# Kernel tuning notes

Hardware: AMD Instinct MI355X
Metric: run time of the kernel (lower is better)

## Reference

```python
import jax, jax.numpy as jnp
import numpy as np

BATCH_SIZE_PER_IM = 512
FG_FRACTION = 0.25
FG_THRESH = 0.5
BG_THRESH_HI = 0.5
BG_THRESH_LO = 0.0
MAX_FG = int(FG_FRACTION * BATCH_SIZE_PER_IM)  # 128


def _rand_boxes(key, shape):
    a = jax.random.uniform(key, shape + (4,), dtype=jnp.float32)
    ymin = jnp.minimum(a[..., 0], a[..., 2])
    ymax = jnp.maximum(a[..., 0], a[..., 2]) + 1e-3
    xmin = jnp.minimum(a[..., 1], a[..., 3])
    xmax = jnp.maximum(a[..., 1], a[..., 3]) + 1e-3
    return jnp.stack([ymin, xmin, ymax, xmax], axis=-1)


def setup_inputs() -> dict:
    key = jax.random.key(0)
    k1, k2, k3, k4 = jax.random.split(key, 4)
    B, N, G = 32, 8192, 128
    boxes = _rand_boxes(k1, (B, N))
    gt_boxes = _rand_boxes(k2, (B, G))
    gt_labels = jax.random.randint(k3, (B, G), 0, 91, dtype=jnp.int32)
    noise = jax.random.uniform(k4, (B, N + G), dtype=jnp.float32)
    return {"boxes": boxes, "gt_boxes": gt_boxes, "gt_labels": gt_labels, "noise": noise}


def _bbox_overlap(boxes, gt_boxes):
    # boxes: [B, M, 4], gt_boxes: [B, G, 4], layout (ymin, xmin, ymax, xmax)
    b_ymin, b_xmin, b_ymax, b_xmax = [boxes[..., i:i + 1] for i in range(4)]  # [B,M,1]
    g_ymin, g_xmin, g_ymax, g_xmax = [gt_boxes[..., i][:, None, :] for i in range(4)]  # [B,1,G]
    i_ymin = jnp.maximum(b_ymin, g_ymin)
    i_xmin = jnp.maximum(b_xmin, g_xmin)
    i_ymax = jnp.minimum(b_ymax, g_ymax)
    i_xmax = jnp.minimum(b_xmax, g_xmax)
    i_area = jnp.maximum(i_ymax - i_ymin, 0.0) * jnp.maximum(i_xmax - i_xmin, 0.0)  # [B,M,G]
    b_area = (b_ymax - b_ymin) * (b_xmax - b_xmin)           # [B,M,1]
    g_area = (g_ymax - g_ymin) * (g_xmax - g_xmin)           # [B,1,G]
    iou = i_area / (b_area + g_area - i_area)
    # padded gt boxes (filled with -1) get IoU = -1
    padding = jnp.logical_and(i_ymin < 0, i_xmin < 0)
    return jnp.where(padding, -1.0, iou)


def reference(boxes, gt_boxes, gt_labels, noise):
    boxes = jax.lax.stop_gradient(boxes)
    all_boxes = jnp.concatenate([boxes, gt_boxes], axis=1)        # [B, M=N+G, 4]
    iou = _bbox_overlap(all_boxes, gt_boxes)                      # [B, M, G]
    max_ov = jnp.max(iou, axis=2)                                 # [B, M]
    p2l = jnp.argmax(iou, axis=2).astype(jnp.int32)               # [B, M]
    box_t = jnp.take_along_axis(gt_boxes, p2l[..., None], axis=1)  # [B, M, 4]
    cls_t = jnp.take_along_axis(gt_labels, p2l, axis=1)           # [B, M]
    pos = max_ov > FG_THRESH
    neg = jnp.logical_and(max_ov >= BG_THRESH_LO, max_ov < BG_THRESH_HI)
    cls_t = jnp.where(neg, 0, cls_t)
    box_t = jnp.where(neg[..., None], 0.0, box_t)
    p2l = jnp.where(neg, 0, p2l)
    # --- balanced fg/bg subsampling (random scores provided in `noise`) ---
    pos_score = jnp.where(pos, noise, -1.0)
    kth = jax.lax.top_k(pos_score, MAX_FG)[0][:, -1:]             # [B,1] threshold
    sel_pos = jnp.logical_and(pos, pos_score >= kth)              # at most MAX_FG fg
    # selected fg get priority band 2+, bg band [0,1), rest -1
    combined = jnp.where(sel_pos, 2.0 + noise, jnp.where(neg, noise, -1.0))
    _, idx = jax.lax.top_k(combined, BATCH_SIZE_PER_IM)           # [B, K]
    rois = jnp.take_along_axis(all_boxes, idx[..., None], axis=1)      # [B, K, 4]
    sample_box_t = jnp.take_along_axis(box_t, idx[..., None], axis=1)  # [B, K, 4]
    sample_cls_t = jnp.take_along_axis(cls_t, idx, axis=1)             # [B, K]
    sample_p2l = jnp.take_along_axis(p2l, idx, axis=1)                 # [B, K]
    return sample_box_t, sample_cls_t, rois, sample_p2l
```

## Files before the change

### kernel.cpp

```cpp
#include <hip/hip_runtime.h>
#include <stdint.h>

#define BATCH 32
#define NBOX 8192
#define NGT 128
#define M (NBOX + NGT)
#define K_OUT 512
#define MAX_FG 128
#define C_CAP 256
#define S_CAP 256
#define U_CAP 1024

#define GSPLIT 2
#define GPER (NGT / GSPLIT)
#define IOU_TPB 256
#define IOU_CB ((M + IOU_TPB - 1) / IOU_TPB)

__device__ __forceinline__ unsigned int bkt1024(float ns) {
    unsigned int u = (unsigned int)(ns * 16777216.0f) >> 14;
    return u > 1023u ? 1023u : u;
}

#define U64KEY(lo, hi) (((unsigned long long)(hi) << 32) | (unsigned long long)(lo))

__global__ __launch_bounds__(256) void iou_kernel(
    const float* __restrict__ boxes,
    const float* __restrict__ gt_boxes,
    unsigned long long* __restrict__ part)
{
    const int s  = blockIdx.x % GSPLIT;
    const int cb = (blockIdx.x / GSPLIT) % IOU_CB;
    const int b  = blockIdx.x / (GSPLIT * IOU_CB);
    const int t  = threadIdx.x;
    const int g0 = s * GPER;

    __shared__ float4 sgt[GPER];
    if (t < GPER)
        sgt[t] = ((const float4*)gt_boxes)[b * NGT + g0 + t];
    __syncthreads();

    const int m = cb * IOU_TPB + t;
    if (m >= M) return;

    float4 bb = (m < NBOX) ? ((const float4*)boxes)[b * NBOX + m]
                           : ((const float4*)gt_boxes)[b * NGT + (m - NBOX)];
    float ba = __fmul_rn(__fsub_rn(bb.z, bb.x), __fsub_rn(bb.w, bb.y));

    float best = -1e30f;
    int bi = 0;
    #pragma unroll 4
    for (int g = 0; g < GPER; ++g) {
        float4 gg = sgt[g];
        float ga = __fmul_rn(__fsub_rn(gg.z, gg.x), __fsub_rn(gg.w, gg.y));
        float iymin = fmaxf(bb.x, gg.x);
        float ixmin = fmaxf(bb.y, gg.y);
        float iymax = fminf(bb.z, gg.z);
        float ixmax = fminf(bb.w, gg.w);
        float ia  = __fmul_rn(fmaxf(__fsub_rn(iymax, iymin), 0.0f),
                              fmaxf(__fsub_rn(ixmax, ixmin), 0.0f));
        float den = __fsub_rn(__fadd_rn(ba, ga), ia);
        float iou = __fdiv_rn(ia, den);
        if (iou > best) { best = iou; bi = g0 + g; }
    }
    part[((size_t)s * BATCH + b) * M + m] =
        U64KEY(127u - (unsigned int)bi, __float_as_uint(best));
}

__device__ __forceinline__ int merged_label(
    const unsigned long long* __restrict__ P0,
    const unsigned long long* __restrict__ P1, int m) {
    unsigned long long ka = P0[m], kb = P1[m];
    unsigned long long kk = ka > kb ? ka : kb;
    return (int)(127u - ((unsigned int)kk & 127u));
}

__global__ __launch_bounds__(1024) void select_kernel(
    const float* __restrict__ boxes,
    const float* __restrict__ gt_boxes,
    const int*   __restrict__ gt_labels,
    const float* __restrict__ noise,
    const unsigned long long* __restrict__ part,
    float* __restrict__ out)
{
    const int b = blockIdx.x;
    const int tid = threadIdx.x;

    __shared__ float sh_ns[M];
    __shared__ unsigned int hist[1024];
    __shared__ unsigned int hist2[1024];
    __shared__ unsigned int bctr[1024];
    __shared__ unsigned short pnmask[M / 8];
    __shared__ float4 sgt[NGT];
    __shared__ int slab[NGT];
    __shared__ float C[C_CAP];
    __shared__ __align__(16) unsigned int   skey[S_CAP + 4];
    __shared__ __align__(16) unsigned short sm[S_CAP + 4];
    __shared__ unsigned int   ukey[U_CAP];
    __shared__ unsigned short um[U_CAP];
    __shared__ unsigned int sh_Bp, sh_needp, sh_cc, sh_n1a, sh_B, sh_kth;

    float* out_bt  = out;
    float* out_cls = out + BATCH * K_OUT * 4;
    float* out_roi = out + BATCH * K_OUT * 5;
    float* out_p2l = out + BATCH * K_OUT * 9;

    const unsigned long long* P0 = part + ((size_t)0 * BATCH + b) * M;
    const unsigned long long* P1 = part + ((size_t)1 * BATCH + b) * M;

    hist[tid] = 0;
    hist2[tid] = 0;
    bctr[tid] = 0;
    if (tid == 0) { sh_cc = 0; sh_n1a = 0; sh_B = 0; sh_kth = 0xBF800000u; }
    if (tid < NGT) {
        sgt[tid]  = ((const float4*)gt_boxes)[b * NGT + tid];
        slab[tid] = gt_labels[b * NGT + tid];
    }
    __syncthreads();

    float f[8];
    unsigned int pb = 0, nb = 0;
    {
        const float4* ns4 = (const float4*)(noise + (size_t)b * M);
        {
            const int c = tid;
            const ulonglong2* a2 = (const ulonglong2*)(P0 + (size_t)c * 8);
            const ulonglong2* b2 = (const ulonglong2*)(P1 + (size_t)c * 8);
            ulonglong2 A0 = a2[0], A1 = a2[1], A2 = a2[2], A3 = a2[3];
            ulonglong2 B0 = b2[0], B1 = b2[1], B2 = b2[2], B3 = b2[3];
            float4 n0 = ns4[2 * c], n1v = ns4[2 * c + 1];
            ((float4*)sh_ns)[2 * c] = n0;
            ((float4*)sh_ns)[2 * c + 1] = n1v;
            f[0] = n0.x; f[1] = n0.y; f[2] = n0.z; f[3] = n0.w;
            f[4] = n1v.x; f[5] = n1v.y; f[6] = n1v.z; f[7] = n1v.w;
            unsigned long long ka[8] = {A0.x, A0.y, A1.x, A1.y,
                                        A2.x, A2.y, A3.x, A3.y};
            unsigned long long kb[8] = {B0.x, B0.y, B1.x, B1.y,
                                        B2.x, B2.y, B3.x, B3.y};
            #pragma unroll
            for (int k = 0; k < 8; ++k) {
                unsigned long long kk = ka[k] > kb[k] ? ka[k] : kb[k];
                unsigned int ub = (unsigned int)(kk >> 32);
                if (ub > 0x3F000000u) {
                    pb |= (1u << k);
                    atomicAdd(&hist2[bkt1024(f[k])], 1u);
                } else if (ub < 0x3F000000u) {
                    nb |= (1u << k);
                    atomicAdd(&hist[bkt1024(f[k])], 1u);
                }
            }
            pnmask[c] = (unsigned short)(pb | (nb << 8));
        }
        if (tid < 16) {
            const int c = 1024 + tid;
            const ulonglong2* a2 = (const ulonglong2*)(P0 + (size_t)c * 8);
            const ulonglong2* b2 = (const ulonglong2*)(P1 + (size_t)c * 8);
            ulonglong2 A0 = a2[0], A1 = a2[1], A2 = a2[2], A3 = a2[3];
            ulonglong2 B0 = b2[0], B1 = b2[1], B2 = b2[2], B3 = b2[3];
            float4 n0 = ns4[2 * c], n1v = ns4[2 * c + 1];
            ((float4*)sh_ns)[2 * c] = n0;
            ((float4*)sh_ns)[2 * c + 1] = n1v;
            float ft[8] = {n0.x, n0.y, n0.z, n0.w, n1v.x, n1v.y, n1v.z, n1v.w};
            unsigned long long ka[8] = {A0.x, A0.y, A1.x, A1.y,
                                        A2.x, A2.y, A3.x, A3.y};
            unsigned long long kb[8] = {B0.x, B0.y, B1.x, B1.y,
                                        B2.x, B2.y, B3.x, B3.y};
            unsigned int pb2 = 0, nb2 = 0;
            #pragma unroll
            for (int k = 0; k < 8; ++k) {
                unsigned long long kk = ka[k] > kb[k] ? ka[k] : kb[k];
                unsigned int ub = (unsigned int)(kk >> 32);
                if (ub > 0x3F000000u) {
                    pb2 |= (1u << k);
                    atomicAdd(&hist2[bkt1024(ft[k])], 1u);
                } else if (ub < 0x3F000000u) {
                    nb2 |= (1u << k);
                    atomicAdd(&hist[bkt1024(ft[k])], 1u);
                }
            }
            pnmask[c] = (unsigned short)(pb2 | (nb2 << 8));
        }
    }
    __syncthreads();

    {
        const int wv = tid >> 6, ln = tid & 63;
        if (wv < 2) {
            unsigned int* H = wv ? hist2 : hist;
            unsigned int s[16];
            #pragma unroll
            for (int k = 0; k < 16; ++k) {
                unsigned int v = H[k * 64 + ln];
                #pragma unroll
                for (int off = 1; off < 64; off <<= 1) {
                    unsigned int o = __shfl_down(v, off, 64);
                    if (ln + off < 64) v += o;
                }
                s[k] = v;
            }
            unsigned int after = 0;
            #pragma unroll
            for (int k = 15; k >= 0; --k) {
                unsigned int tot = __shfl(s[k], 0, 64);
                H[k * 64 + ln] = s[k] + after;
                after += tot;
            }
        }
    }
    __syncthreads();
    const unsigned int nneg = hist[0];
    const unsigned int npos = hist2[0];

    if (npos >= MAX_FG) {
        {
            unsigned int S  = hist2[tid];
            unsigned int Sn = (tid < 1023) ? hist2[tid + 1] : 0;
            if (S >= MAX_FG && Sn < MAX_FG) { sh_Bp = tid; sh_needp = MAX_FG - Sn; }
        }
        __syncthreads();
        const unsigned int Bp = sh_Bp, needp = sh_needp;
        #pragma unroll
        for (int k = 0; k < 8; ++k) {
            if (((pb >> k) & 1u) && bkt1024(f[k]) == Bp) {
                unsigned int slot = atomicAdd(&sh_cc, 1u);
                if (slot < C_CAP) C[slot] = f[k];
            }
        }
        if (tid < 16) {
            unsigned int pb2 = pnmask[1024 + tid] & 0xFFu;
            #pragma unroll
            for (int k = 0; k < 8; ++k) {
                if ((pb2 >> k) & 1u) {
                    float v = sh_ns[(1024 + tid) * 8 + k];
                    if (bkt1024(v) == Bp) {
                        unsigned int slot = atomicAdd(&sh_cc, 1u);
                        if (slot < C_CAP) C[slot] = v;
                    }
                }
            }
        }
        __syncthreads();
        {
            unsigned int cc = min(sh_cc, (unsigned int)C_CAP);
            if (tid < (int)cc) {
                float my = C[tid];
                unsigned int g = 0, e = 0;
                for (unsigned int j = 0; j < cc; ++j) {
                    float v = C[j];
                    g += (v > my) ? 1u : 0u;
                    e += (v == my) ? 1u : 0u;
                }
                if (g < needp && g + e >= needp) sh_kth = __float_as_uint(my);
            }
        }
        __syncthreads();
    }
    const float kthf = __uint_as_float(sh_kth);

    #pragma unroll
    for (int k = 0; k < 8; ++k) {
        if (((pb >> k) & 1u) && f[k] >= kthf) {
            unsigned int slot = atomicAdd(&sh_n1a, 1u);
            if (slot < S_CAP) {
                skey[slot] = __float_as_uint(__fadd_rn(2.0f, f[k]));
                sm[slot]   = (unsigned short)(tid * 8 + k);
            }
        }
    }
    if (tid < 16) {
        unsigned int pb2 = pnmask[1024 + tid] & 0xFFu;
        #pragma unroll
        for (int k = 0; k < 8; ++k) {
            if ((pb2 >> k) & 1u) {
                int m = (1024 + tid) * 8 + k;
                float v = sh_ns[m];
                if (v >= kthf) {
                    unsigned int slot = atomicAdd(&sh_n1a, 1u);
                    if (slot < S_CAP) {
                        skey[slot] = __float_as_uint(__fadd_rn(2.0f, v));
                        sm[slot]   = (unsigned short)m;
                    }
                }
            }
        }
    }
    __syncthreads();
    const unsigned int n1 = min(sh_n1a, (unsigned int)S_CAP);
    const unsigned int k2 = K_OUT - n1;
    const bool enough_neg = (nneg >= k2);

    if (tid < 4) { skey[n1 + tid] = 0u; sm[n1 + tid] = 0xFFFFu; }
    if (enough_neg) {
        unsigned int S  = hist[tid];
        unsigned int Sn = (tid < 1023) ? hist[tid + 1] : 0;
        if (S >= k2 && Sn < k2) sh_B = tid;
    }
    __syncthreads();
    const unsigned int B1 = sh_B;

    if (tid < (int)n1) {
        unsigned int   ki = skey[tid];
        unsigned short mi = sm[tid];
        unsigned int r = 0;
        for (unsigned int j = 0; j < n1; j += 4) {
            uint4   kv = *(const uint4*)&skey[j];
            ushort4 mv = *(const ushort4*)&sm[j];
            r += (kv.x > ki || (kv.x == ki && mv.x < mi)) ? 1u : 0u;
            r += (kv.y > ki || (kv.y == ki && mv.y < mi)) ? 1u : 0u;
            r += (kv.z > ki || (kv.z == ki && mv.z < mi)) ? 1u : 0u;
            r += (kv.w > ki || (kv.w == ki && mv.w < mi)) ? 1u : 0u;
        }
        int mi_ = mi;
        int lbl = merged_label(P0, P1, mi_);
        float4 roi = (mi_ < NBOX) ? ((const float4*)boxes)[b * NBOX + mi_]
                                  : sgt[mi_ - NBOX];
        ((float4*)out_bt)[b * K_OUT + r] = sgt[lbl];
        out_cls[b * K_OUT + r] = (float)slab[lbl];
        ((float4*)out_roi)[b * K_OUT + r] = roi;
        out_p2l[b * K_OUT + r] = (float)lbl;
    }

    #pragma unroll
    for (int k = 0; k < 8; ++k) {
        if ((nb >> k) & 1u) {
            float v = f[k];
            unsigned int be = bkt1024(v);
            if (be >= B1) {
                unsigned int base = (be < 1023) ? hist[be + 1] : 0;
                unsigned int a = base + atomicAdd(&bctr[be], 1u);
                if (a < U_CAP) {
                    ukey[a] = __float_as_uint(v);
                    um[a]   = (unsigned short)(tid * 8 + k);
                }
            }
        }
    }
    if (tid < 16) {
        unsigned int nb2 = (pnmask[1024 + tid] >> 8) & 0xFFu;
        #pragma unroll
        for (int k = 0; k < 8; ++k) {
            if ((nb2 >> k) & 1u) {
                int m = (1024 + tid) * 8 + k;
                float v = sh_ns[m];
                unsigned int be = bkt1024(v);
                if (be >= B1) {
                    unsigned int base = (be < 1023) ? hist[be + 1] : 0;
                    unsigned int a = base + atomicAdd(&bctr[be], 1u);
                    if (a < U_CAP) {
                        ukey[a] = __float_as_uint(v);
                        um[a]   = (unsigned short)m;
                    }
                }
            }
        }
    }
    __syncthreads();

    const unsigned int q = min(hist[B1], (unsigned int)U_CAP);
    for (unsigned int a = tid; a < q; a += 1024) {
        unsigned int   ki = ukey[a];
        unsigned short mi = um[a];
        unsigned int be = bkt1024(__uint_as_float(ki));
        unsigned int base = (be < 1023) ? hist[be + 1] : 0;
        unsigned int end  = min(hist[be], q);
        unsigned int r = base;
        for (unsigned int j = base; j < end; ++j) {
            unsigned int kj = ukey[j];
            if (kj > ki || (kj == ki && um[j] < mi)) ++r;
        }
        if (r < k2) {
            float4 roi = (mi < NBOX) ? ((const float4*)boxes)[b * NBOX + mi]
                                     : sgt[mi - NBOX];
            unsigned int gr = n1 + r;
            ((float4*)out_bt)[b * K_OUT + gr] = make_float4(0.f, 0.f, 0.f, 0.f);
            out_cls[b * K_OUT + gr] = 0.0f;
            ((float4*)out_roi)[b * K_OUT + gr] = roi;
            out_p2l[b * K_OUT + gr] = 0.0f;
        }
    }

    if (!enough_neg) {
        __syncthreads();
        const unsigned int k3 = k2 - nneg;
        for (int m = tid; m < M; m += 1024) {
            if (((pnmask[m >> 3] >> (m & 7)) & 1) && sh_ns[m] < kthf) {
                unsigned int r = 0;
                for (int m2 = 0; m2 < m; ++m2)
                    if (((pnmask[m2 >> 3] >> (m2 & 7)) & 1) && sh_ns[m2] < kthf) ++r;
                if (r < k3) {
                    int lbl = merged_label(P0, P1, m);
                    float4 roi = (m < NBOX) ? ((const float4*)boxes)[b * NBOX + m]
                                            : sgt[m - NBOX];
                    unsigned int gr = n1 + nneg + r;
                    ((float4*)out_bt)[b * K_OUT + gr] = sgt[lbl];
                    out_cls[b * K_OUT + gr] = (float)slab[lbl];
                    ((float4*)out_roi)[b * K_OUT + gr] = roi;
                    out_p2l[b * K_OUT + gr] = (float)lbl;
                }
            }
        }
    }
}

extern "C" void kernel_launch(void* const* d_in, const int* in_sizes, int n_in,
                              void* d_out, int out_size, void* d_ws, size_t ws_size,
                              hipStream_t stream) {
    const float* boxes     = (const float*)d_in[0];
    const float* gt_boxes  = (const float*)d_in[1];
    const int*   gt_labels = (const int*)d_in[2];
    const float* noise     = (const float*)d_in[3];
    unsigned long long* part = (unsigned long long*)d_ws;
    float* out = (float*)d_out;

    iou_kernel<<<BATCH * IOU_CB * GSPLIT, IOU_TPB, 0, stream>>>(boxes, gt_boxes, part);
    select_kernel<<<BATCH, 1024, 0, stream>>>(boxes, gt_boxes, gt_labels, noise,
                                              part, out);
}
```

Before: 108.6 us.

## Move fg/bg classification and histogram building into a wide separate kernel

The per-box merge of the two IoU partial maxima, the fg/bg classification and the noise histograms are moved out of the 32-block select kernel into a new classify kernel spread across the whole GPU. That kernel writes global histograms, with atomics, and per-chunk masks. The iou kernel zeroes the global histograms first. The select kernel then only loads the precomputed histograms and masks, which removes the large shared-memory noise buffer and the serial classification work done by only 32 blocks. In exchange it adds a kernel launch, contended global atomics, and global-memory reads in the rare fallback path.

```diff
diff --git a/kernel.cpp b/kernel.cpp
--- a/kernel.cpp
+++ b/kernel.cpp
@@ -5,6 +5,7 @@
 #define NBOX 8192
 #define NGT 128
 #define M (NBOX + NGT)
+#define NCH (M / 8)
 #define K_OUT 512
 #define MAX_FG 128
 #define C_CAP 256
@@ -16,6 +17,8 @@
 #define IOU_TPB 256
 #define IOU_CB ((M + IOU_TPB - 1) / IOU_TPB)
 
+#define TH_HALF 0x3F000000u
+
 __device__ __forceinline__ unsigned int bkt1024(float ns) {
     unsigned int u = (unsigned int)(ns * 16777216.0f) >> 14;
     return u > 1023u ? 1023u : u;
@@ -26,8 +29,12 @@
 __global__ __launch_bounds__(256) void iou_kernel(
     const float* __restrict__ boxes,
     const float* __restrict__ gt_boxes,
-    unsigned long long* __restrict__ part)
+    unsigned long long* __restrict__ part,
+    unsigned int* __restrict__ hist_g)
 {
+    if (blockIdx.x < 256)
+        hist_g[blockIdx.x * 256 + threadIdx.x] = 0;
+
     const int s  = blockIdx.x % GSPLIT;
     const int cb = (blockIdx.x / GSPLIT) % IOU_CB;
     const int b  = blockIdx.x / (GSPLIT * IOU_CB);
@@ -66,6 +73,55 @@
         U64KEY(127u - (unsigned int)bi, __float_as_uint(best));
 }
 
+__global__ __launch_bounds__(256) void classify_kernel(
+    const unsigned long long* __restrict__ part,
+    const float* __restrict__ noise,
+    unsigned int* __restrict__ hist_g,
+    unsigned short* __restrict__ pn_g)
+{
+    const int c  = blockIdx.x * 256 + threadIdx.x;
+    const int b  = c / NCH;
+    const int cl = c - b * NCH;
+    const int m0 = cl * 8;
+
+    const unsigned long long* P0 = part + ((size_t)0 * BATCH + b) * M + m0;
+    const unsigned long long* P1 = part + ((size_t)1 * BATCH + b) * M + m0;
+    const float4* ns4 = (const float4*)(noise + (size_t)b * M + m0);
+
+    ulonglong2 A0 = ((const ulonglong2*)P0)[0], A1 = ((const ulonglong2*)P0)[1];
+    ulonglong2 A2 = ((const ulonglong2*)P0)[2], A3 = ((const ulonglong2*)P0)[3];
+    ulonglong2 B0 = ((const ulonglong2*)P1)[0], B1 = ((const ulonglong2*)P1)[1];
+    ulonglong2 B2 = ((const ulonglong2*)P1)[2], B3 = ((const ulonglong2*)P1)[3];
+    float4 n0 = ns4[0], n1v = ns4[1];
+
+    unsigned int ha[8] = {
+        (unsigned int)(A0.x >> 32), (unsigned int)(A0.y >> 32),
+        (unsigned int)(A1.x >> 32), (unsigned int)(A1.y >> 32),
+        (unsigned int)(A2.x >> 32), (unsigned int)(A2.y >> 32),
+        (unsigned int)(A3.x >> 32), (unsigned int)(A3.y >> 32)};
+    unsigned int hb[8] = {
+        (unsigned int)(B0.x >> 32), (unsigned int)(B0.y >> 32),
+        (unsigned int)(B1.x >> 32), (unsigned int)(B1.y >> 32),
+        (unsigned int)(B2.x >> 32), (unsigned int)(B2.y >> 32),
+        (unsigned int)(B3.x >> 32), (unsigned int)(B3.y >> 32)};
+    float f[8] = {n0.x, n0.y, n0.z, n0.w, n1v.x, n1v.y, n1v.z, n1v.w};
+
+    unsigned int* hg = hist_g + b * 2048;
+    unsigned int pb = 0, nb = 0;
+    #pragma unroll
+    for (int k = 0; k < 8; ++k) {
+        unsigned int ub = ha[k] > hb[k] ? ha[k] : hb[k];
+        if (ub > TH_HALF) {
+            pb |= (1u << k);
+            atomicAdd(&hg[1024 + bkt1024(f[k])], 1u);
+        } else if (ub < TH_HALF) {
+            nb |= (1u << k);
+            atomicAdd(&hg[bkt1024(f[k])], 1u);
+        }
+    }
+    pn_g[c] = (unsigned short)(pb | (nb << 8));
+}
+
 __device__ __forceinline__ int merged_label(
     const unsigned long long* __restrict__ P0,
     const unsigned long long* __restrict__ P1, int m) {
@@ -80,16 +136,17 @@
     const int*   __restrict__ gt_labels,
     const float* __restrict__ noise,
     const unsigned long long* __restrict__ part,
+    const unsigned int* __restrict__ hist_g,
+    const unsigned short* __restrict__ pn_g,
     float* __restrict__ out)
 {
     const int b = blockIdx.x;
     const int tid = threadIdx.x;
 
-    __shared__ float sh_ns[M];
+    __shared__ float sh_ns_t[128];
     __shared__ unsigned int hist[1024];
     __shared__ unsigned int hist2[1024];
     __shared__ unsigned int bctr[1024];
-    __shared__ unsigned short pnmask[M / 8];
     __shared__ float4 sgt[NGT];
     __shared__ int slab[NGT];
     __shared__ float C[C_CAP];
@@ -106,79 +163,27 @@
 
     const unsigned long long* P0 = part + ((size_t)0 * BATCH + b) * M;
     const unsigned long long* P1 = part + ((size_t)1 * BATCH + b) * M;
-
-    hist[tid] = 0;
-    hist2[tid] = 0;
-    bctr[tid] = 0;
-    if (tid == 0) { sh_cc = 0; sh_n1a = 0; sh_B = 0; sh_kth = 0xBF800000u; }
-    if (tid < NGT) {
-        sgt[tid]  = ((const float4*)gt_boxes)[b * NGT + tid];
-        slab[tid] = gt_labels[b * NGT + tid];
-    }
-    __syncthreads();
+    const unsigned short* pn = pn_g + (size_t)b * NCH;
 
     float f[8];
-    unsigned int pb = 0, nb = 0;
+    unsigned int pb, nb;
     {
         const float4* ns4 = (const float4*)(noise + (size_t)b * M);
-        {
-            const int c = tid;
-            const ulonglong2* a2 = (const ulonglong2*)(P0 + (size_t)c * 8);
-            const ulonglong2* b2 = (const ulonglong2*)(P1 + (size_t)c * 8);
-            ulonglong2 A0 = a2[0], A1 = a2[1], A2 = a2[2], A3 = a2[3];
-            ulonglong2 B0 = b2[0], B1 = b2[1], B2 = b2[2], B3 = b2[3];
-            float4 n0 = ns4[2 * c], n1v = ns4[2 * c + 1];
-            ((float4*)sh_ns)[2 * c] = n0;
-            ((float4*)sh_ns)[2 * c + 1] = n1v;
-            f[0] = n0.x; f[1] = n0.y; f[2] = n0.z; f[3] = n0.w;
-            f[4] = n1v.x; f[5] = n1v.y; f[6] = n1v.z; f[7] = n1v.w;
-            unsigned long long ka[8] = {A0.x, A0.y, A1.x, A1.y,
-                                        A2.x, A2.y, A3.x, A3.y};
-            unsigned long long kb[8] = {B0.x, B0.y, B1.x, B1.y,
-                                        B2.x, B2.y, B3.x, B3.y};
-            #pragma unroll
-            for (int k = 0; k < 8; ++k) {
-                unsigned long long kk = ka[k] > kb[k] ? ka[k] : kb[k];
-                unsigned int ub = (unsigned int)(kk >> 32);
-                if (ub > 0x3F000000u) {
-                    pb |= (1u << k);
-                    atomicAdd(&hist2[bkt1024(f[k])], 1u);
-                } else if (ub < 0x3F000000u) {
-                    nb |= (1u << k);
-                    atomicAdd(&hist[bkt1024(f[k])], 1u);
-                }
-            }
-            pnmask[c] = (unsigned short)(pb | (nb << 8));
-        }
-        if (tid < 16) {
-            const int c = 1024 + tid;
-            const ulonglong2* a2 = (const ulonglong2*)(P0 + (size_t)c * 8);
-            const ulonglong2* b2 = (const ulonglong2*)(P1 + (size_t)c * 8);
-            ulonglong2 A0 = a2[0], A1 = a2[1], A2 = a2[2], A3 = a2[3];
-            ulonglong2 B0 = b2[0], B1 = b2[1], B2 = b2[2], B3 = b2[3];
-            float4 n0 = ns4[2 * c], n1v = ns4[2 * c + 1];
-            ((float4*)sh_ns)[2 * c] = n0;
-            ((float4*)sh_ns)[2 * c + 1] = n1v;
-            float ft[8] = {n0.x, n0.y, n0.z, n0.w, n1v.x, n1v.y, n1v.z, n1v.w};
-            unsigned long long ka[8] = {A0.x, A0.y, A1.x, A1.y,
-                                        A2.x, A2.y, A3.x, A3.y};
-            unsigned long long kb[8] = {B0.x, B0.y, B1.x, B1.y,
-                                        B2.x, B2.y, B3.x, B3.y};
-            unsigned int pb2 = 0, nb2 = 0;
-            #pragma unroll
-            for (int k = 0; k < 8; ++k) {
-                unsigned long long kk = ka[k] > kb[k] ? ka[k] : kb[k];
-                unsigned int ub = (unsigned int)(kk >> 32);
-                if (ub > 0x3F000000u) {
-                    pb2 |= (1u << k);
-                    atomicAdd(&hist2[bkt1024(ft[k])], 1u);
-                } else if (ub < 0x3F000000u) {
-                    nb2 |= (1u << k);
-                    atomicAdd(&hist[bkt1024(ft[k])], 1u);
-                }
-            }
-            pnmask[c] = (unsigned short)(pb2 | (nb2 << 8));
-        }
+        float4 n0 = ns4[2 * tid], n1v = ns4[2 * tid + 1];
+        f[0] = n0.x; f[1] = n0.y; f[2] = n0.z; f[3] = n0.w;
+        f[4] = n1v.x; f[5] = n1v.y; f[6] = n1v.z; f[7] = n1v.w;
+        unsigned int pnv = pn[tid];
+        pb = pnv & 0xFFu;
+        nb = (pnv >> 8) & 0xFFu;
+        hist[tid]  = hist_g[b * 2048 + tid];
+        hist2[tid] = hist_g[b * 2048 + 1024 + tid];
+        bctr[tid] = 0;
+        if (tid < 128) sh_ns_t[tid] = noise[(size_t)b * M + NBOX + tid];
+        if (tid < NGT) {
+            sgt[tid]  = ((const float4*)gt_boxes)[b * NGT + tid];
+            slab[tid] = gt_labels[b * NGT + tid];
+        }
+        if (tid == 0) { sh_cc = 0; sh_n1a = 0; sh_B = 0; sh_kth = 0xBF800000u; }
     }
     __syncthreads();
 
@@ -226,11 +231,11 @@
             }
         }
         if (tid < 16) {
-            unsigned int pb2 = pnmask[1024 + tid] & 0xFFu;
+            unsigned int pb2 = pn[1024 + tid] & 0xFFu;
             #pragma unroll
             for (int k = 0; k < 8; ++k) {
                 if ((pb2 >> k) & 1u) {
-                    float v = sh_ns[(1024 + tid) * 8 + k];
+                    float v = sh_ns_t[tid * 8 + k];
                     if (bkt1024(v) == Bp) {
                         unsigned int slot = atomicAdd(&sh_cc, 1u);
                         if (slot < C_CAP) C[slot] = v;
@@ -267,17 +272,16 @@
         }
     }
     if (tid < 16) {
-        unsigned int pb2 = pnmask[1024 + tid] & 0xFFu;
+        unsigned int pb2 = pn[1024 + tid] & 0xFFu;
         #pragma unroll
         for (int k = 0; k < 8; ++k) {
             if ((pb2 >> k) & 1u) {
-                int m = (1024 + tid) * 8 + k;
-                float v = sh_ns[m];
+                float v = sh_ns_t[tid * 8 + k];
                 if (v >= kthf) {
                     unsigned int slot = atomicAdd(&sh_n1a, 1u);
                     if (slot < S_CAP) {
                         skey[slot] = __float_as_uint(__fadd_rn(2.0f, v));
-                        sm[slot]   = (unsigned short)m;
+                        sm[slot]   = (unsigned short)((1024 + tid) * 8 + k);
                     }
                 }
             }
@@ -335,19 +339,18 @@
         }
     }
     if (tid < 16) {
-        unsigned int nb2 = (pnmask[1024 + tid] >> 8) & 0xFFu;
+        unsigned int nb2 = (pn[1024 + tid] >> 8) & 0xFFu;
         #pragma unroll
         for (int k = 0; k < 8; ++k) {
             if ((nb2 >> k) & 1u) {
-                int m = (1024 + tid) * 8 + k;
-                float v = sh_ns[m];
+                float v = sh_ns_t[tid * 8 + k];
                 unsigned int be = bkt1024(v);
                 if (be >= B1) {
                     unsigned int base = (be < 1023) ? hist[be + 1] : 0;
                     unsigned int a = base + atomicAdd(&bctr[be], 1u);
                     if (a < U_CAP) {
                         ukey[a] = __float_as_uint(v);
-                        um[a]   = (unsigned short)m;
+                        um[a]   = (unsigned short)((1024 + tid) * 8 + k);
                     }
                 }
             }
@@ -381,11 +384,12 @@
     if (!enough_neg) {
         __syncthreads();
         const unsigned int k3 = k2 - nneg;
+        const float* nsb = noise + (size_t)b * M;
         for (int m = tid; m < M; m += 1024) {
-            if (((pnmask[m >> 3] >> (m & 7)) & 1) && sh_ns[m] < kthf) {
+            if (((pn[m >> 3] >> (m & 7)) & 1) && nsb[m] < kthf) {
                 unsigned int r = 0;
                 for (int m2 = 0; m2 < m; ++m2)
-                    if (((pnmask[m2 >> 3] >> (m2 & 7)) & 1) && sh_ns[m2] < kthf) ++r;
+                    if (((pn[m2 >> 3] >> (m2 & 7)) & 1) && nsb[m2] < kthf) ++r;
                 if (r < k3) {
                     int lbl = merged_label(P0, P1, m);
                     float4 roi = (m < NBOX) ? ((const float4*)boxes)[b * NBOX + m]
@@ -408,10 +412,16 @@
     const float* gt_boxes  = (const float*)d_in[1];
     const int*   gt_labels = (const int*)d_in[2];
     const float* noise     = (const float*)d_in[3];
+    float* out = (float*)d_out;
+
     unsigned long long* part = (unsigned long long*)d_ws;
-    float* out = (float*)d_out;
-
-    iou_kernel<<<BATCH * IOU_CB * GSPLIT, IOU_TPB, 0, stream>>>(boxes, gt_boxes, part);
-    select_kernel<<<BATCH, 1024, 0, stream>>>(boxes, gt_boxes, gt_labels, noise,
-                                              part, out);
-}
+    unsigned int* hist_g = (unsigned int*)((char*)d_ws + 4259840);
+    unsigned short* pn_g = (unsigned short*)((char*)d_ws + 4521984);
+
+    iou_kernel<<<BATCH * IOU_CB * GSPLIT, IOU_TPB, 0, stream>>>(
+        boxes, gt_boxes, part, hist_g);
+    classify_kernel<<<(BATCH * NCH) / 256, 256, 0, stream>>>(
+        part, noise, hist_g, pn_g);
+    select_kernel<<<BATCH, 1024, 0, stream>>>(
+        boxes, gt_boxes, gt_labels, noise, part, hist_g, pn_g, out);
+}
```

Result: slower. 115.8 us (+6.7%).
